# Kernel optimization log

Measured on AMD Instinct MI355X. Metric: run time of the kernel, lower is better.

The kernel has to match this reference:

```python
import jax, jax.numpy as jnp
import numpy as np

B, N, D = 2, 2048, 1024
H = 16
HD = D // H


def setup_inputs() -> dict:
    key = jax.random.key(0)
    ks = jax.random.split(key, 10)
    s = 1.0 / np.sqrt(D)
    return {
        "x": jax.random.normal(ks[0], (B, N, D), dtype=jnp.float32),
        "B_gaussian": jax.random.normal(ks[1], (B, N, N), dtype=jnp.float32),
        "Wq": jax.random.normal(ks[2], (D, D), dtype=jnp.float32) * s,
        "bq": jnp.zeros((D,), dtype=jnp.float32),
        "Wk": jax.random.normal(ks[3], (D, D), dtype=jnp.float32) * s,
        "bk": jnp.zeros((D,), dtype=jnp.float32),
        "Wv": jax.random.normal(ks[4], (D, D), dtype=jnp.float32) * s,
        "bv": jnp.zeros((D,), dtype=jnp.float32),
        "Wo": jax.random.normal(ks[5], (D, D), dtype=jnp.float32) * s,
        "bo": jnp.zeros((D,), dtype=jnp.float32),
        "lam": jnp.float32(0.5),
    }


def reference(x, B_gaussian, Wq, bq, Wk, bk, Wv, bv, Wo, bo, lam):
    b, n, d = x.shape
    # project and split heads: [b, h, n, hd]
    def heads(W, bias):
        return (x @ W + bias).reshape(b, n, H, HD).transpose(0, 2, 1, 3)
    q = heads(Wq, bq)
    k = heads(Wk, bk)
    v = heads(Wv, bv)
    scale = 1.0 / np.sqrt(HD)
    # scores [b, h, n, n] with Gaussian bias broadcast across heads
    scores = jnp.einsum("bhid,bhjd->bhij", q, k) * scale + lam * B_gaussian[:, None, :, :]
    w = jax.nn.softmax(scores, axis=-1)
    out = jnp.einsum("bhij,bhjd->bhid", w, v)
    out = out.transpose(0, 2, 1, 3).reshape(b, n, d)
    return out @ Wo + bo
```

## Files before the change

### kernel.cpp

```cpp
#include <hip/hip_runtime.h>
#include <math.h>
#include <stdint.h>

namespace {
constexpr int kB  = 2;
constexpr int kN  = 2048;
constexpr int kD  = 1024;
constexpr int kH  = 16;
constexpr int kM  = kB * kN;
}

typedef __attribute__((ext_vector_type(8))) _Float16 f16x8;
typedef __attribute__((ext_vector_type(2))) __fp16   fp16x2;
typedef __attribute__((ext_vector_type(4))) float    f32x4;

__device__ __forceinline__ void split16(float v, _Float16& h, _Float16& l) {
    h = (_Float16)v;
    l = (_Float16)(v - (float)h);
}

__device__ __forceinline__ void gl2lds16(const _Float16* g, _Float16* l) {
    __builtin_amdgcn_global_load_lds(
        (const __attribute__((address_space(1))) void*)g,
        (__attribute__((address_space(3))) void*)l, 16, 0, 0);
}

__global__ __launch_bounds__(256)
void cvt16(const float* __restrict__ x, _Float16* __restrict__ o)
{
    const size_t i = ((size_t)blockIdx.x * 256 + threadIdx.x) * 8;
    const float4 a = *(const float4*)(x + i);
    const float4 b = *(const float4*)(x + i + 4);
    _Float16 h[8] = {(_Float16)a.x, (_Float16)a.y, (_Float16)a.z, (_Float16)a.w,
                     (_Float16)b.x, (_Float16)b.y, (_Float16)b.z, (_Float16)b.w};
    *(uint4*)(o + i) = *(uint4*)h;
}

__global__ __launch_bounds__(256)
void bgprep(const float* __restrict__ Bg, const float* __restrict__ lam_p,
            _Float16* __restrict__ bgC)
{
    const int t    = blockIdx.x * 256 + threadIdx.x;
    const int lane = t & 63;
    const int i16  = (t >> 6) & 127;
    const int jt   = (t >> 13) & 31;
    const int b    = t >> 18;
    const int q    = lane >> 4;
    const int m    = lane & 15;
    const float c  = lam_p[0] * 8.0f;
    const float* src = Bg + ((size_t)b * kN + i16 * 16 + m) * kN + jt * 64 + q * 4;
    _Float16 h[16];
#pragma unroll
    for (int js = 0; js < 4; ++js) {
        const float4 v = *(const float4*)(src + js * 16);
        h[js * 4 + 0] = (_Float16)(c * v.x);
        h[js * 4 + 1] = (_Float16)(c * v.y);
        h[js * 4 + 2] = (_Float16)(c * v.z);
        h[js * 4 + 3] = (_Float16)(c * v.w);
    }
    _Float16* dst = bgC + (size_t)t * 16;
    *(uint4*)(dst)     = *(uint4*)(h);
    *(uint4*)(dst + 8) = *(uint4*)(h + 8);
}

__global__ __launch_bounds__(256)
void wcvt_t(const float* __restrict__ W, _Float16* __restrict__ Ot)
{
    __shared__ float sT[64][69];
    const int tid = threadIdx.x;
    const int k0 = blockIdx.x << 6;
    const int n0 = blockIdx.y << 6;
#pragma unroll
    for (int rep = 0; rep < 4; ++rep) {
        const int idx = tid + (rep << 8);
        const int kr  = idx >> 4;
        const int c4  = (idx & 15) << 2;
        const float4 v = *(const float4*)(W + (size_t)(k0 + kr) * kD + n0 + c4);
        sT[kr][c4 + 0] = v.x; sT[kr][c4 + 1] = v.y;
        sT[kr][c4 + 2] = v.z; sT[kr][c4 + 3] = v.w;
    }
    __syncthreads();
#pragma unroll
    for (int rep = 0; rep < 2; ++rep) {
        const int slot = tid + (rep << 8);
        const int n  = slot >> 3;
        const int k8 = (slot & 7) << 3;
        _Float16 h8[8];
#pragma unroll
        for (int j = 0; j < 8; ++j) h8[j] = (_Float16)sT[k8 + j][n];
        *(uint4*)(Ot + (size_t)(n0 + n) * kD + k0 + k8) = *(uint4*)h8;
    }
}

__global__ __launch_bounds__(256)
void wsplit_t(const float* __restrict__ W, _Float16* __restrict__ Oh,
              _Float16* __restrict__ Ol)
{
    __shared__ float sT[64][69];
    const int tid = threadIdx.x;
    const int k0 = blockIdx.x << 6;
    const int n0 = blockIdx.y << 6;
#pragma unroll
    for (int rep = 0; rep < 4; ++rep) {
        const int idx = tid + (rep << 8);
        const int kr  = idx >> 4;
        const int c4  = (idx & 15) << 2;
        const float4 v = *(const float4*)(W + (size_t)(k0 + kr) * kD + n0 + c4);
        sT[kr][c4 + 0] = v.x; sT[kr][c4 + 1] = v.y;
        sT[kr][c4 + 2] = v.z; sT[kr][c4 + 3] = v.w;
    }
    __syncthreads();
#pragma unroll
    for (int rep = 0; rep < 2; ++rep) {
        const int slot = tid + (rep << 8);
        const int n  = slot >> 3;
        const int k8 = (slot & 7) << 3;
        _Float16 h8[8], l8[8];
#pragma unroll
        for (int j = 0; j < 8; ++j) split16(sT[k8 + j][n], h8[j], l8[j]);
        *(uint4*)(Oh + (size_t)(n0 + n) * kD + k0 + k8) = *(uint4*)h8;
        *(uint4*)(Ol + (size_t)(n0 + n) * kD + k0 + k8) = *(uint4*)l8;
    }
}

__global__ __launch_bounds__(256)
void gemm16(const _Float16* __restrict__ A, const _Float16* __restrict__ Bt,
            const _Float16* __restrict__ Btl,
            const float* __restrict__ b0, const float* __restrict__ b1,
            const float* __restrict__ b2,
            _Float16* __restrict__ Qf, _Float16* __restrict__ Kf,
            _Float16* __restrict__ Vt, float* __restrict__ outF, int mode)
{
    extern __shared__ _Float16 dyn[];
    _Float16* sA  = dyn;
    _Float16* sB  = dyn + 128 * 64;
    _Float16* sBl = dyn + 2 * 128 * 64;

    const int tid  = threadIdx.x;
    const int lane = tid & 63;
    const int w    = tid >> 6;
    const int quad = lane >> 4;
    const int m16  = lane & 15;
    const int wrow = (w >> 1) << 6;
    const int wcol = (w & 1) << 6;

    const int row0 = blockIdx.y << 7;
    const int col0 = blockIdx.x << 7;

    f32x4 acc[4][4];
#pragma unroll
    for (int mr = 0; mr < 4; ++mr)
#pragma unroll
        for (int nr = 0; nr < 4; ++nr) acc[mr][nr] = (f32x4){0.f, 0.f, 0.f, 0.f};

    const int srl = lane >> 3;
    const int sg  = lane & 7;

    auto stage = [&](const _Float16* gsrc, _Float16* ldst) {
#pragma unroll
        for (int t = 0; t < 4; ++t) {
            const int rr = (w << 5) + (t << 3);
            const int r  = rr + srl;
            const int gg = (sg ^ (r & 7)) << 3;
            gl2lds16(gsrc + (size_t)r * kD + gg, ldst + rr * 64);
        }
    };

    for (int kt = 0; kt < 16; ++kt) {
        const int k0 = kt << 6;
        stage(A  + (size_t)row0 * kD + k0, sA);
        stage(Bt + (size_t)col0 * kD + k0, sB);
        if (mode == 1) stage(Btl + (size_t)col0 * kD + k0, sBl);
        __syncthreads();

#pragma unroll
        for (int ks = 0; ks < 2; ++ks) {
            const int sw = (((ks << 2) | quad) ^ (m16 & 7)) << 3;
            f16x8 af[4], bf[4], blf[4];
#pragma unroll
            for (int mr = 0; mr < 4; ++mr)
                af[mr] = *(const f16x8*)(sA + (wrow + mr * 16 + m16) * 64 + sw);
#pragma unroll
            for (int nr = 0; nr < 4; ++nr) {
                const int off = (wcol + nr * 16 + m16) * 64 + sw;
                bf[nr] = *(const f16x8*)(sB + off);
                if (mode == 1) blf[nr] = *(const f16x8*)(sBl + off);
            }
#pragma unroll
            for (int mr = 0; mr < 4; ++mr)
#pragma unroll
                for (int nr = 0; nr < 4; ++nr) {
                    acc[mr][nr] = __builtin_amdgcn_mfma_f32_16x16x32_f16(af[mr], bf[nr], acc[mr][nr], 0, 0, 0);
                    if (mode == 1)
                        acc[mr][nr] = __builtin_amdgcn_mfma_f32_16x16x32_f16(af[mr], blf[nr], acc[mr][nr], 0, 0, 0);
                }
        }
        __syncthreads();
    }

    if (mode == 1) {
#pragma unroll
        for (int mr = 0; mr < 4; ++mr)
#pragma unroll
            for (int nr = 0; nr < 4; ++nr)
#pragma unroll
                for (int r = 0; r < 4; ++r) {
                    const int row = row0 + wrow + mr * 16 + quad * 4 + r;
                    const int col = col0 + wcol + nr * 16 + m16;
                    outF[(size_t)row * kD + col] = acc[mr][nr][r] + b0[col];
                }
        return;
    }

    const float* bias; int cb; _Float16* dst = nullptr; bool vmode = false;
    if (col0 < 1024)      { bias = b0; cb = col0;        dst = Qf; }
    else if (col0 < 2048) { bias = b1; cb = col0 - 1024; dst = Kf; }
    else                  { bias = b2; cb = col0 - 2048; vmode = true; }

    _Float16* T = dyn;

    if (!vmode) {
#pragma unroll
        for (int mr = 0; mr < 4; ++mr)
#pragma unroll
            for (int nr = 0; nr < 4; ++nr)
#pragma unroll
                for (int r = 0; r < 4; ++r) {
                    const int row = wrow + mr * 16 + quad * 4 + r;
                    const int cl  = wcol + nr * 16 + m16;
                    T[row * 136 + cl] = (_Float16)(acc[mr][nr][r] + bias[cb + cl]);
                }
        __syncthreads();
#pragma unroll
        for (int rep = 0; rep < 8; ++rep) {
            const int slot = tid + (rep << 8);
            const int row = slot >> 4;
            const int c8  = (slot & 15) << 3;
            *(uint4*)(dst + (size_t)(row0 + row) * kD + cb + c8) =
                *(const uint4*)(T + row * 136 + c8);
        }
    } else {
#pragma unroll
        for (int mr = 0; mr < 4; ++mr)
#pragma unroll
            for (int nr = 0; nr < 4; ++nr)
#pragma unroll
                for (int r = 0; r < 4; ++r) {
                    const int tok  = wrow + mr * 16 + quad * 4 + r;
                    const int tokP = (tok & 64) | (tok & 32) |
                                     (((tok >> 2) & 3) << 3) |
                                     (((tok >> 4) & 1) << 2) | (tok & 3);
                    const int cl   = wcol + nr * 16 + m16;
                    T[cl * 136 + tokP] = (_Float16)(acc[mr][nr][r] + bias[cb + cl]);
                }
        __syncthreads();
        const int b  = row0 >> 11;
        const int n0 = row0 & (kN - 1);
#pragma unroll
        for (int rep = 0; rep < 8; ++rep) {
            const int slot = tid + (rep << 8);
            const int cl = slot >> 4;
            const int t8 = (slot & 15) << 3;
            *(uint4*)(Vt + ((size_t)(b * kD + cb + cl)) * kN + n0 + t8) =
                *(const uint4*)(T + cl * 136 + t8);
        }
    }
}

#define LOADT(JT, KP0, KP1, VP0, VP1, BG0, BG1, BG2, BG3)                      \
    {                                                                          \
        const int j0_ = (JT) << 6;                                             \
        KP0 = *(const uint4*)(Kf + (size_t)(b * kN + j0_ + srow) * kD + h * 64 + sc8);      \
        KP1 = *(const uint4*)(Kf + (size_t)(b * kN + j0_ + srow + 32) * kD + h * 64 + sc8); \
        VP0 = *(const uint4*)(Vt + (size_t)(b * kD + h * 64 + srow) * kN + j0_ + sc8);      \
        VP1 = *(const uint4*)(Vt + (size_t)(b * kD + h * 64 + srow + 32) * kN + j0_ + sc8); \
        const _Float16* bp0_ = bgbase0 + (size_t)(JT) * kBgJt;                 \
        const _Float16* bp1_ = bgbase1 + (size_t)(JT) * kBgJt;                 \
        BG0 = *(const f16x8*)(bp0_);                                           \
        BG1 = *(const f16x8*)(bp0_ + 8);                                       \
        BG2 = *(const f16x8*)(bp1_);                                           \
        BG3 = *(const f16x8*)(bp1_ + 8);                                       \
    }

#define STAGET(BUF, KP0, KP1, VP0, VP1)                                        \
    {                                                                          \
        *(uint4*)&sK[BUF][srow][sc8]      = KP0;                               \
        *(uint4*)&sK[BUF][srow + 32][sc8] = KP1;                               \
        *(uint4*)&sV[BUF][srow][sc8]      = VP0;                               \
        *(uint4*)&sV[BUF][srow + 32][sc8] = VP1;                               \
    }

#define PHASE(BUF, BG0, BG1, BG2, BG3)                                         \
    {                                                                          \
        f32x4 sacc[2][4];                                                      \
        _Pragma("unroll")                                                      \
        for (int r = 0; r < 4; ++r) {                                          \
            sacc[0][0][r] = (float)BG0[r];                                     \
            sacc[0][1][r] = (float)BG0[4 + r];                                 \
            sacc[0][2][r] = (float)BG1[r];                                     \
            sacc[0][3][r] = (float)BG1[4 + r];                                 \
            sacc[1][0][r] = (float)BG2[r];                                     \
            sacc[1][1][r] = (float)BG2[4 + r];                                 \
            sacc[1][2][r] = (float)BG3[r];                                     \
            sacc[1][3][r] = (float)BG3[4 + r];                                 \
        }                                                                      \
        __builtin_amdgcn_s_setprio(1);                                         \
        _Pragma("unroll")                                                      \
        for (int ks = 0; ks < 2; ++ks)                                         \
            _Pragma("unroll")                                                  \
            for (int js = 0; js < 4; ++js) {                                   \
                const f16x8 kf = *(const f16x8*)&sK[BUF][js * 16 + m16][ks * 32 + quad * 8];            \
                sacc[0][js] = __builtin_amdgcn_mfma_f32_16x16x32_f16(kf, qf[0][ks], sacc[0][js], 0, 0, 0); \
                sacc[1][js] = __builtin_amdgcn_mfma_f32_16x16x32_f16(kf, qf[1][ks], sacc[1][js], 0, 0, 0); \
            }                                                                  \
        __builtin_amdgcn_s_setprio(0);                                         \
        union { f16x8 v; unsigned u[4]; } pf[2][2];                            \
        _Pragma("unroll")                                                      \
        for (int iq = 0; iq < 2; ++iq)                                         \
            _Pragma("unroll")                                                  \
            for (int js = 0; js < 4; ++js) {                                   \
                const float p0 = __expf(fmaf(sacc[iq][js][0], 0.125f, -4.0f)); \
                const float p1 = __expf(fmaf(sacc[iq][js][1], 0.125f, -4.0f)); \
                const float p2 = __expf(fmaf(sacc[iq][js][2], 0.125f, -4.0f)); \
                const float p3 = __expf(fmaf(sacc[iq][js][3], 0.125f, -4.0f)); \
                lsum[iq] += (p0 + p1) + (p2 + p3);                             \
                union { fp16x2 h; unsigned u; } ua_, ub_;                      \
                ua_.h = __builtin_amdgcn_cvt_pkrtz(p0, p1);                    \
                ub_.h = __builtin_amdgcn_cvt_pkrtz(p2, p3);                    \
                pf[iq][js >> 1].u[(js & 1) * 2 + 0] = ua_.u;                   \
                pf[iq][js >> 1].u[(js & 1) * 2 + 1] = ub_.u;                   \
            }                                                                  \
        __builtin_amdgcn_s_setprio(1);                                         \
        _Pragma("unroll")                                                      \
        for (int ks = 0; ks < 2; ++ks)                                         \
            _Pragma("unroll")                                                  \
            for (int ds = 0; ds < 4; ++ds) {                                   \
                const f16x8 vf = *(const f16x8*)&sV[BUF][ds * 16 + m16][ks * 32 + quad * 8];            \
                O[0][ds] = __builtin_amdgcn_mfma_f32_16x16x32_f16(pf[0][ks].v, vf, O[0][ds], 0, 0, 0);  \
                O[1][ds] = __builtin_amdgcn_mfma_f32_16x16x32_f16(pf[1][ks].v, vf, O[1][ds], 0, 0, 0);  \
            }                                                                  \
        __builtin_amdgcn_s_setprio(0);                                         \
    }

__global__ __launch_bounds__(256, 2)
void attn_f16(const _Float16* __restrict__ Qf, const _Float16* __restrict__ Kf,
              const _Float16* __restrict__ Vt, const _Float16* __restrict__ BgC,
              _Float16* __restrict__ AOh)
{
    __shared__ _Float16 sK[2][64][72];
    __shared__ _Float16 sV[2][64][72];

    const int tid  = threadIdx.x;
    const int lane = tid & 63;
    const int w    = tid >> 6;
    const int quad = lane >> 4;
    const int m16  = lane & 15;

    const int bh = blockIdx.x;
    const int qt = blockIdx.y;
    const int b  = bh >> 4;
    const int h  = bh & 15;
    const int i0 = qt << 7;

    f16x8 qf[2][2];
#pragma unroll
    for (int iq = 0; iq < 2; ++iq) {
        const size_t qoff =
            (size_t)(b * kN + i0 + iq * 64 + w * 16 + m16) * kD + h * 64 + quad * 8;
        qf[iq][0] = *(const f16x8*)(Qf + qoff);
        qf[iq][1] = *(const f16x8*)(Qf + qoff + 32);
    }

    f32x4 O[2][4];
#pragma unroll
    for (int iq = 0; iq < 2; ++iq)
#pragma unroll
        for (int ds = 0; ds < 4; ++ds) O[iq][ds] = (f32x4){0.f, 0.f, 0.f, 0.f};
    float lsum[2] = {0.f, 0.f};

    const int srow = tid >> 3;
    const int sc8  = (tid & 7) << 3;

    const _Float16* bgbase0 =
        BgC + (((size_t)b * 32 * 128 + (qt * 8 + w)) * 64 + lane) * 16;
    const _Float16* bgbase1 = bgbase0 + (size_t)4 * 64 * 16;
    constexpr size_t kBgJt = (size_t)128 * 64 * 16;

    uint4 kpA0, kpA1, vpA0, vpA1, kpB0, kpB1, vpB0, vpB1;
    f16x8 bgA0, bgA1, bgA2, bgA3, bgB0, bgB1, bgB2, bgB3;

    LOADT(0, kpA0, kpA1, vpA0, vpA1, bgA0, bgA1, bgA2, bgA3);
    STAGET(0, kpA0, kpA1, vpA0, vpA1);
    LOADT(1, kpB0, kpB1, vpB0, vpB1, bgB0, bgB1, bgB2, bgB3);
    __syncthreads();

    for (int t = 0; t < kN / 64; t += 2) {
        PHASE(0, bgA0, bgA1, bgA2, bgA3);
        if (t + 2 < kN / 64)
            LOADT(t + 2, kpA0, kpA1, vpA0, vpA1, bgA0, bgA1, bgA2, bgA3);
        STAGET(1, kpB0, kpB1, vpB0, vpB1);
        __syncthreads();

        PHASE(1, bgB0, bgB1, bgB2, bgB3);
        if (t + 3 < kN / 64)
            LOADT(t + 3, kpB0, kpB1, vpB0, vpB1, bgB0, bgB1, bgB2, bgB3);
        if (t + 2 < kN / 64)
            STAGET(0, kpA0, kpA1, vpA0, vpA1);
        __syncthreads();
    }

#pragma unroll
    for (int iq = 0; iq < 2; ++iq) {
        float l = lsum[iq];
        l += __shfl_xor(l, 16, 64);
        l += __shfl_xor(l, 32, 64);

        const int orow = b * kN + i0 + iq * 64 + w * 16 + quad * 4;
#pragma unroll
        for (int r = 0; r < 4; ++r) {
            const float inv = 1.0f / __shfl(l, quad * 4 + r, 64);
#pragma unroll
            for (int ds = 0; ds < 4; ++ds)
                AOh[(size_t)(orow + r) * kD + h * 64 + ds * 16 + m16] =
                    (_Float16)(O[iq][ds][r] * inv);
        }
    }
}

extern "C" void kernel_launch(void* const* d_in, const int* in_sizes, int n_in,
                              void* d_out, int out_size, void* d_ws, size_t ws_size,
                              hipStream_t stream)
{
    (void)in_sizes; (void)n_in; (void)out_size; (void)ws_size;

    const float* x   = (const float*)d_in[0];
    const float* Bg  = (const float*)d_in[1];
    const float* Wq  = (const float*)d_in[2];
    const float* bq  = (const float*)d_in[3];
    const float* Wk  = (const float*)d_in[4];
    const float* bk  = (const float*)d_in[5];
    const float* Wv  = (const float*)d_in[6];
    const float* bv  = (const float*)d_in[7];
    const float* Wo  = (const float*)d_in[8];
    const float* bo  = (const float*)d_in[9];
    const float* lam = (const float*)d_in[10];
    float* out = (float*)d_out;
    _Float16* ws16 = (_Float16*)d_ws;

    constexpr size_t kQKV = (size_t)kM * kD;
    constexpr size_t kW   = (size_t)kD * kD;
    _Float16* Qf   = ws16;
    _Float16* Kf   = ws16 + 1 * kQKV;
    _Float16* Vt   = ws16 + 2 * kQKV;
    _Float16* x16  = ws16 + 3 * kQKV;
    _Float16* AOh  = x16;
    _Float16* Wt3  = ws16 + 4 * kQKV;
    _Float16* Woth = Wt3 + 3 * kW;
    _Float16* Wotl = Woth + kW;
    _Float16* BgC  = Wotl + kW;

    dim3 blk(256);

    cvt16<<<dim3(2048), blk, 0, stream>>>(x, x16);
    bgprep<<<dim3(2048), blk, 0, stream>>>(Bg, lam, BgC);
    dim3 wg(kD / 64, kD / 64);
    wcvt_t  <<<wg, blk, 0, stream>>>(Wq, Wt3);
    wcvt_t  <<<wg, blk, 0, stream>>>(Wk, Wt3 + kW);
    wcvt_t  <<<wg, blk, 0, stream>>>(Wv, Wt3 + 2 * kW);
    wsplit_t<<<wg, blk, 0, stream>>>(Wo, Woth, Wotl);

    gemm16<<<dim3(3 * kD / 128, kM / 128), blk, 34816, stream>>>(
        x16, Wt3, nullptr, bq, bk, bv, Qf, Kf, Vt, nullptr, 0);

    attn_f16<<<dim3(kB * kH, kN / 128), dim3(256), 0, stream>>>(
        Qf, Kf, Vt, BgC, AOh);

    gemm16<<<dim3(kD / 128, kM / 128), blk, 49152, stream>>>(
        AOh, Woth, Wotl, bo, nullptr, nullptr,
        nullptr, nullptr, nullptr, out, 1);
}
```

Before: 260.6 us.

## Split attention KV loop across two wave groups with LDS reduction

The attention kernel grows from 256 to 512 threads. The two 4-wave groups each process alternating 64-key tiles: even tiles for one group, odd tiles for the other, so each group runs half as many loop iterations. Group 1 writes its partial O accumulators and row sums to LDS, and group 0 adds them in and normalizes before the output store. This aims to raise occupancy and latency hiding per query tile, at the cost of doubled LDS buffers, an extra reduction step and tighter register limits from launch_bounds(512,4).

After: 548.6 us. +110.5%, slower.

```diff
diff --git a/kernel.cpp b/kernel.cpp
--- a/kernel.cpp
+++ b/kernel.cpp
@@ -284,10 +284,10 @@
 
 #define STAGET(BUF, KP0, KP1, VP0, VP1)                                        \
     {                                                                          \
-        *(uint4*)&sK[BUF][srow][sc8]      = KP0;                               \
-        *(uint4*)&sK[BUF][srow + 32][sc8] = KP1;                               \
-        *(uint4*)&sV[BUF][srow][sc8]      = VP0;                               \
-        *(uint4*)&sV[BUF][srow + 32][sc8] = VP1;                               \
+        *(uint4*)&sK[grp][BUF][srow][sc8]      = KP0;                          \
+        *(uint4*)&sK[grp][BUF][srow + 32][sc8] = KP1;                          \
+        *(uint4*)&sV[grp][BUF][srow][sc8]      = VP0;                          \
+        *(uint4*)&sV[grp][BUF][srow + 32][sc8] = VP1;                          \
     }
 
 #define PHASE(BUF, BG0, BG1, BG2, BG3)                                         \
@@ -309,7 +309,7 @@
         for (int ks = 0; ks < 2; ++ks)                                         \
             _Pragma("unroll")                                                  \
             for (int js = 0; js < 4; ++js) {                                   \
-                const f16x8 kf = *(const f16x8*)&sK[BUF][js * 16 + m16][ks * 32 + quad * 8];            \
+                const f16x8 kf = *(const f16x8*)&sK[grp][BUF][js * 16 + m16][ks * 32 + quad * 8];       \
                 sacc[0][js] = __builtin_amdgcn_mfma_f32_16x16x32_f16(kf, qf[0][ks], sacc[0][js], 0, 0, 0); \
                 sacc[1][js] = __builtin_amdgcn_mfma_f32_16x16x32_f16(kf, qf[1][ks], sacc[1][js], 0, 0, 0); \
             }                                                                  \
@@ -335,24 +335,26 @@
         for (int ks = 0; ks < 2; ++ks)                                         \
             _Pragma("unroll")                                                  \
             for (int ds = 0; ds < 4; ++ds) {                                   \
-                const f16x8 vf = *(const f16x8*)&sV[BUF][ds * 16 + m16][ks * 32 + quad * 8];            \
+                const f16x8 vf = *(const f16x8*)&sV[grp][BUF][ds * 16 + m16][ks * 32 + quad * 8];       \
                 O[0][ds] = __builtin_amdgcn_mfma_f32_16x16x32_f16(pf[0][ks].v, vf, O[0][ds], 0, 0, 0);  \
                 O[1][ds] = __builtin_amdgcn_mfma_f32_16x16x32_f16(pf[1][ks].v, vf, O[1][ds], 0, 0, 0);  \
             }                                                                  \
         __builtin_amdgcn_s_setprio(0);                                         \
     }
 
-__global__ __launch_bounds__(256, 2)
+__global__ __launch_bounds__(512, 4)
 void attn_f16(const _Float16* __restrict__ Qf, const _Float16* __restrict__ Kf,
               const _Float16* __restrict__ Vt, const _Float16* __restrict__ BgC,
               _Float16* __restrict__ AOh)
 {
-    __shared__ _Float16 sK[2][64][72];
-    __shared__ _Float16 sV[2][64][72];
+    __shared__ _Float16 sK[2][2][64][72];
+    __shared__ _Float16 sV[2][2][64][72];
 
     const int tid  = threadIdx.x;
     const int lane = tid & 63;
     const int w    = tid >> 6;
+    const int grp  = w >> 2;
+    const int wg   = w & 3;
     const int quad = lane >> 4;
     const int m16  = lane & 15;
 
@@ -366,7 +368,7 @@
 #pragma unroll
     for (int iq = 0; iq < 2; ++iq) {
         const size_t qoff =
-            (size_t)(b * kN + i0 + iq * 64 + w * 16 + m16) * kD + h * 64 + quad * 8;
+            (size_t)(b * kN + i0 + iq * 64 + wg * 16 + m16) * kD + h * 64 + quad * 8;
         qf[iq][0] = *(const f16x8*)(Qf + qoff);
         qf[iq][1] = *(const f16x8*)(Qf + qoff + 32);
     }
@@ -378,51 +380,75 @@
         for (int ds = 0; ds < 4; ++ds) O[iq][ds] = (f32x4){0.f, 0.f, 0.f, 0.f};
     float lsum[2] = {0.f, 0.f};
 
-    const int srow = tid >> 3;
-    const int sc8  = (tid & 7) << 3;
+    const int gtid = tid & 255;
+    const int srow = gtid >> 3;
+    const int sc8  = (gtid & 7) << 3;
 
     const _Float16* bgbase0 =
-        BgC + (((size_t)b * 32 * 128 + (qt * 8 + w)) * 64 + lane) * 16;
+        BgC + (((size_t)b * 32 * 128 + (qt * 8 + wg)) * 64 + lane) * 16;
     const _Float16* bgbase1 = bgbase0 + (size_t)4 * 64 * 16;
     constexpr size_t kBgJt = (size_t)128 * 64 * 16;
 
     uint4 kpA0, kpA1, vpA0, vpA1, kpB0, kpB1, vpB0, vpB1;
     f16x8 bgA0, bgA1, bgA2, bgA3, bgB0, bgB1, bgB2, bgB3;
 
-    LOADT(0, kpA0, kpA1, vpA0, vpA1, bgA0, bgA1, bgA2, bgA3);
+    LOADT(grp, kpA0, kpA1, vpA0, vpA1, bgA0, bgA1, bgA2, bgA3);
     STAGET(0, kpA0, kpA1, vpA0, vpA1);
-    LOADT(1, kpB0, kpB1, vpB0, vpB1, bgB0, bgB1, bgB2, bgB3);
+    LOADT(2 + grp, kpB0, kpB1, vpB0, vpB1, bgB0, bgB1, bgB2, bgB3);
     __syncthreads();
 
-    for (int t = 0; t < kN / 64; t += 2) {
+    for (int t = 0; t < 16; t += 2) {
         PHASE(0, bgA0, bgA1, bgA2, bgA3);
-        if (t + 2 < kN / 64)
-            LOADT(t + 2, kpA0, kpA1, vpA0, vpA1, bgA0, bgA1, bgA2, bgA3);
+        if (t + 2 < 16)
+            LOADT(2 * (t + 2) + grp, kpA0, kpA1, vpA0, vpA1, bgA0, bgA1, bgA2, bgA3);
         STAGET(1, kpB0, kpB1, vpB0, vpB1);
         __syncthreads();
 
         PHASE(1, bgB0, bgB1, bgB2, bgB3);
-        if (t + 3 < kN / 64)
-            LOADT(t + 3, kpB0, kpB1, vpB0, vpB1, bgB0, bgB1, bgB2, bgB3);
-        if (t + 2 < kN / 64)
+        if (t + 3 < 16)
+            LOADT(2 * (t + 3) + grp, kpB0, kpB1, vpB0, vpB1, bgB0, bgB1, bgB2, bgB3);
+        if (t + 2 < 16)
             STAGET(0, kpA0, kpA1, vpA0, vpA1);
         __syncthreads();
     }
 
-#pragma unroll
-    for (int iq = 0; iq < 2; ++iq) {
-        float l = lsum[iq];
-        l += __shfl_xor(l, 16, 64);
-        l += __shfl_xor(l, 32, 64);
-
-        const int orow = b * kN + i0 + iq * 64 + w * 16 + quad * 4;
-#pragma unroll
-        for (int r = 0; r < 4; ++r) {
-            const float inv = 1.0f / __shfl(l, quad * 4 + r, 64);
+    float* fbuf = (float*)&sK[0][0][0][0];
+    if (grp == 1) {
+#pragma unroll
+        for (int iq = 0; iq < 2; ++iq)
 #pragma unroll
             for (int ds = 0; ds < 4; ++ds)
-                AOh[(size_t)(orow + r) * kD + h * 64 + ds * 16 + m16] =
-                    (_Float16)(O[iq][ds][r] * inv);
+                *(f32x4*)&fbuf[gtid * 36 + (iq * 4 + ds) * 4] = O[iq][ds];
+        fbuf[gtid * 36 + 32] = lsum[0];
+        fbuf[gtid * 36 + 33] = lsum[1];
+    }
+    __syncthreads();
+    if (grp == 0) {
+#pragma unroll
+        for (int iq = 0; iq < 2; ++iq) {
+#pragma unroll
+            for (int ds = 0; ds < 4; ++ds) {
+                const f32x4 o2 = *(const f32x4*)&fbuf[gtid * 36 + (iq * 4 + ds) * 4];
+                O[iq][ds] += o2;
+            }
+            lsum[iq] += fbuf[gtid * 36 + 32 + iq];
+        }
+
+#pragma unroll
+        for (int iq = 0; iq < 2; ++iq) {
+            float l = lsum[iq];
+            l += __shfl_xor(l, 16, 64);
+            l += __shfl_xor(l, 32, 64);
+
+            const int orow = b * kN + i0 + iq * 64 + wg * 16 + quad * 4;
+#pragma unroll
+            for (int r = 0; r < 4; ++r) {
+                const float inv = 1.0f / __shfl(l, quad * 4 + r, 64);
+#pragma unroll
+                for (int ds = 0; ds < 4; ++ds)
+                    AOh[(size_t)(orow + r) * kD + h * 64 + ds * 16 + m16] =
+                        (_Float16)(O[iq][ds][r] * inv);
+            }
         }
     }
 }
@@ -472,7 +498,7 @@
     gemm16<<<dim3(3 * kD / 128, kM / 128), blk, 34816, stream>>>(
         x16, Wt3, nullptr, bq, bk, bv, Qf, Kf, Vt, nullptr, 0);
 
-    attn_f16<<<dim3(kB * kH, kN / 128), dim3(256), 0, stream>>>(
+    attn_f16<<<dim3(kB * kH, kN / 128), dim3(512), 0, stream>>>(
         Qf, Kf, Vt, BgC, AOh);
 
     gemm16<<<dim3(kD / 128, kM / 128), blk, 49152, stream>>>(
```
